# Kernel optimization log

Measured on AMD Instinct MI355X. Metric: run time of the kernel, lower is better.

Reference implementation:

```python
import jax, jax.numpy as jnp
import numpy as np

B, S, H = 4, 8192, 576
I = 512   # moe_intermediate_size
E = 8     # num routed experts
TOP_K = 2

def setup_inputs() -> dict:
    key = jax.random.key(0)
    ks = jax.random.split(key, 8)
    sc = lambda fan_in: 1.0 / np.sqrt(fan_in)
    return {
        'x': jax.random.normal(ks[0], (B, S, H), dtype=jnp.float32),
        'shared_gate_w': jax.random.normal(ks[1], (H, I), dtype=jnp.float32) * sc(H),
        'shared_up_w':   jax.random.normal(ks[2], (H, I), dtype=jnp.float32) * sc(H),
        'shared_down_w': jax.random.normal(ks[3], (I, H), dtype=jnp.float32) * sc(I),
        'routed_gate_w': jax.random.normal(ks[4], (E, H, I), dtype=jnp.float32) * sc(H),
        'routed_up_w':   jax.random.normal(ks[5], (E, H, I), dtype=jnp.float32) * sc(H),
        'routed_down_w': jax.random.normal(ks[6], (E, I, H), dtype=jnp.float32) * sc(I),
        'router_w':      jax.random.normal(ks[7], (H, E), dtype=jnp.float32) * sc(H),
        'router_bias':   jnp.zeros((E,), dtype=jnp.float32),
    }

def reference(x, shared_gate_w, shared_up_w, shared_down_w,
              routed_gate_w, routed_up_w, routed_down_w,
              router_w, router_bias):
    b, s, h = x.shape
    flat = x.reshape(-1, h)                               # [T, H]
    T = flat.shape[0]

    # shared expert (SwiGLU)
    shared = (jax.nn.silu(flat @ shared_gate_w) * (flat @ shared_up_w)) @ shared_down_w

    # router: softmax over experts, top-k, renormalize, scatter back to dense weights
    router_logits = flat @ router_w + router_bias          # [T, E]
    routing_weights = jax.nn.softmax(router_logits, axis=1)
    topk_w, topk_i = jax.lax.top_k(routing_weights, TOP_K)  # [T, k]
    topk_w = topk_w / jnp.sum(topk_w, axis=-1, keepdims=True)
    expert_weights = jnp.zeros((T, routing_weights.shape[1]), dtype=routing_weights.dtype)
    expert_weights = expert_weights.at[jnp.arange(T)[:, None], topk_i].set(topk_w)

    # dense all-expert SwiGLU (faithful to reference: every token through every expert)
    gate = jnp.einsum('th,ehi->tei', flat, routed_gate_w)   # [T, E, I]
    up   = jnp.einsum('th,ehi->tei', flat, routed_up_w)
    expert_out = jnp.einsum('tei,eih->teh', jax.nn.silu(gate) * up, routed_down_w)  # [T, E, H]

    weighted = jnp.einsum('teh,te->th', expert_out, expert_weights)
    return (shared + weighted).reshape(b, s, h)
```

## Files before the change

### kernel.cpp

```cpp
#include <hip/hip_runtime.h>
#include <stdint.h>

#define T_TOK 32768
#define H_DIM 576
#define I_DIM 512
#define NEXP 8
#define WELEM 294912

#define NB_RT 512
#define NB_CW 7776

typedef __attribute__((ext_vector_type(8))) short short8;
typedef __attribute__((ext_vector_type(4))) float f32x4;
typedef __attribute__((ext_vector_type(4))) float f4;
typedef __attribute__((ext_vector_type(4))) unsigned short u16x4;

__device__ __forceinline__ unsigned short f2bf(float f) {
  union { float f; unsigned u; } v; v.f = f;
  unsigned r = (v.u + 0x7fffu + ((v.u >> 16) & 1u)) >> 16;
  return (unsigned short)r;
}

__device__ __forceinline__ void gl16(const void* g, void* l) {
  __builtin_amdgcn_global_load_lds(
      (const __attribute__((address_space(1))) unsigned*)g,
      (__attribute__((address_space(3))) unsigned*)l, 16, 0, 0);
}

__global__ __launch_bounds__(256) void prep_k(
    const float* __restrict__ x, unsigned short* __restrict__ xb,
    const float* __restrict__ rw, const float* __restrict__ rb,
    int* __restrict__ tki, float* __restrict__ tkw, int* __restrict__ counts,
    const float* __restrict__ sgw, const float* __restrict__ suw,
    const float* __restrict__ rgw, const float* __restrict__ ruw,
    const float* __restrict__ sdw, const float* __restrict__ rdw,
    unsigned short* __restrict__ wsg, unsigned short* __restrict__ wsu,
    unsigned short* __restrict__ wrg, unsigned short* __restrict__ wru,
    unsigned short* __restrict__ wsd, unsigned short* __restrict__ wrd) {
  __shared__ __align__(16) char smem[29312];
  int b = blockIdx.x, tid = threadIdx.x;
  if (b < NB_RT) {
    float* lrw = (float*)smem;
    float (*tile)[68] = (float(*)[68])(smem + 18432);
    float (*red)[8] = (float(*)[8])(smem + 27136);
    int* hist = (int*)(smem + 29184);
    for (int i = tid; i < 1152; i += 256)
      *(f4*)&lrw[i * 4] = *(const f4*)&rw[i * 4];
    if (tid < 16) hist[tid] = 0;
    int t0 = b * 64;
    float acc[NEXP] = {};
    for (int c = 0; c < 18; c++) {
      __syncthreads();
#pragma unroll
      for (int k = 0; k < 2; k++) {
        int f = tid + k * 256;
        int rgrp = f >> 8, fl = f & 255;
        int tl2 = fl >> 2, seg = fl & 3;
        int h = rgrp * 288 + c * 16 + seg * 4;
        size_t gi = (size_t)(t0 + tl2) * H_DIM + h;
        f4 v = *(const f4*)(x + gi);
        u16x4 o;
        o.x = f2bf(v.x); o.y = f2bf(v.y); o.z = f2bf(v.z); o.w = f2bf(v.w);
        *(u16x4*)(xb + gi) = o;
        int row = rgrp * 16 + seg * 4;
        tile[row + 0][tl2] = v.x; tile[row + 1][tl2] = v.y;
        tile[row + 2][tl2] = v.z; tile[row + 3][tl2] = v.w;
      }
      __syncthreads();
      if (tid < 128) {
        int half = tid >> 6, tl = tid & 63;
        int hbase = half * 288 + c * 16;
        int rbase = half * 16;
#pragma unroll
        for (int hh = 0; hh < 16; hh++) {
          float xv = tile[rbase + hh][tl];
          f4 w0 = *(const f4*)&lrw[(hbase + hh) * 8];
          f4 w1 = *(const f4*)&lrw[(hbase + hh) * 8 + 4];
          acc[0] += xv * w0.x; acc[1] += xv * w0.y;
          acc[2] += xv * w0.z; acc[3] += xv * w0.w;
          acc[4] += xv * w1.x; acc[5] += xv * w1.y;
          acc[6] += xv * w1.z; acc[7] += xv * w1.w;
        }
      }
    }
    if (tid >= 64 && tid < 128) {
      int tl = tid & 63;
#pragma unroll
      for (int e = 0; e < NEXP; e++) red[tl][e] = acc[e];
    }
    __syncthreads();
    if (tid < 64) {
      int t = t0 + tid;
      float l[NEXP];
#pragma unroll
      for (int e = 0; e < NEXP; e++) l[e] = acc[e] + red[tid][e] + rb[e];
      int e0 = 0;
#pragma unroll
      for (int e = 1; e < NEXP; e++) if (l[e] > l[e0]) e0 = e;
      int e1 = -1;
#pragma unroll
      for (int e = 0; e < NEXP; e++) {
        if (e == e0) continue;
        if (e1 < 0 || l[e] > l[e1]) e1 = e;
      }
      float w0 = 1.f / (1.f + __expf(l[e1] - l[e0]));
      tki[t * 2] = e0; tki[t * 2 + 1] = e1;
      tkw[t * 2] = w0; tkw[t * 2 + 1] = 1.f - w0;
      atomicAdd(&hist[e0], 1);
      atomicAdd(&hist[8 + e1], 1);
    }
    __syncthreads();
    if (tid < 16) atomicAdd(&counts[tid * 32], hist[tid]);
  } else {
    float (*tile)[33] = (float(*)[33])smem;
    int b0 = b - NB_RT;
    const float* src; unsigned short* dst;
    int C, bx, by;
    if (b0 < 5184) {
      int z = b0 / 288, r = b0 % 288;
      bx = r & 15; by = r >> 4; C = 512;
      if (z == 0)      { src = sgw;                            dst = wsg; }
      else if (z == 1) { src = suw;                            dst = wsu; }
      else if (z < 10) { src = rgw + (size_t)(z - 2) * WELEM;  dst = wrg + (size_t)(z - 2) * WELEM; }
      else             { src = ruw + (size_t)(z - 10) * WELEM; dst = wru + (size_t)(z - 10) * WELEM; }
    } else {
      int b2 = b0 - 5184;
      int z = b2 / 288, r = b2 % 288;
      bx = r % 18; by = r / 18; C = 576;
      src = (z == 0) ? sdw : rdw + (size_t)(z - 1) * WELEM;
      dst = (z == 0) ? wsd : wrd + (size_t)(z - 1) * WELEM;
    }
    int R = 1088 - C;
    int tx = tid & 31, ty = tid >> 5;
    int r0 = by * 32, c0 = bx * 32;
    for (int i = ty; i < 32; i += 8)
      tile[i][tx] = src[(size_t)(r0 + i) * C + c0 + tx];
    __syncthreads();
    for (int i = ty; i < 32; i += 8)
      dst[(size_t)(c0 + i) * R + r0 + tx] = f2bf(tile[tx][i]);
  }
}

__global__ void offsets_k(const int* __restrict__ counts, int* __restrict__ offs16,
                          int* __restrict__ pcnt16, int* __restrict__ pinfo) {
  if (threadIdx.x == 0) {
    int o = 0;
    for (int s = 0; s < 16; s++) {
      int c = counts[s * 32];
      int pc = (c + 127) & ~127;
      offs16[s] = o; pcnt16[s] = pc;
      o += pc;
    }
    pinfo[0] = offs16[8];
    pinfo[1] = o - offs16[8];
  }
}

__global__ __launch_bounds__(256) void scatter_k(
    const int* __restrict__ tki, const float* __restrict__ tkw,
    const int* __restrict__ offs16, int* __restrict__ cursor ,
    int* __restrict__ etok, float* __restrict__ ew) {
  __shared__ int hist[16], base[16], lcur[16];
  int tid = threadIdx.x;
  if (tid < 16) { hist[tid] = 0; lcur[tid] = 0; }
  __syncthreads();
  int t = blockIdx.x * 256 + tid;
  int s0 = tki[t * 2], s1 = 8 + tki[t * 2 + 1];
  atomicAdd(&hist[s0], 1);
  atomicAdd(&hist[s1], 1);
  __syncthreads();
  if (tid < 16) base[tid] = atomicAdd(&cursor[tid * 32], hist[tid]);
  __syncthreads();
#pragma unroll
  for (int k = 0; k < 2; k++) {
    int s = (k == 0) ? s0 : s1;
    int r = atomicAdd(&lcur[s], 1);
    int slot = offs16[s] + base[s] + r;
    etok[slot] = t;
    ew[slot] = tkw[t * 2 + k];
  }
}

template <int SHARED>
__global__ __launch_bounds__(512, 2) void gateup_k(
    const unsigned short* __restrict__ xb, const unsigned short* __restrict__ wg,
    const unsigned short* __restrict__ wu, unsigned short* __restrict__ h,
    const int* __restrict__ etok, const int* __restrict__ offs16,
    const int* __restrict__ pcnt16, const int* __restrict__ pinfo,
    int p, int merged, int mchunk) {
  int bid = blockIdx.x;
  int xcd = bid & 7, l = bid >> 3;
  int mb = xcd * mchunk + (l >> 2);
  int nb = l & 3;
  int nrows = SHARED ? T_TOK : (merged ? pinfo[0] + pinfo[1] : pinfo[p]);
  if (mb * 128 >= nrows) return;
  __shared__ unsigned short As[128 * 32];
  __shared__ unsigned short Bg[128 * 32];
  __shared__ unsigned short Bu[128 * 32];
  int t = threadIdx.x;
  int wv = t >> 6, lane = t & 63;
  int ar = t >> 2, seg = t & 3;
  int sg = seg ^ ((ar >> 1) & 3);
  int m0 = mb * 128 + ar;
  int tok0, e = 0;
  if (SHARED) {
    tok0 = m0;
  } else {
    int rl = (!merged && p) ? pinfo[0] : 0;
    int g = rl + m0;
    int s = 0;
#pragma unroll
    for (int i = 0; i < 15; i++) s += (g >= offs16[i] + pcnt16[i]) ? 1 : 0;
    e = s & 7;
    tok0 = etok[g];
    if (tok0 < 0) tok0 = 0;
  }
  const unsigned short* ga = xb + (size_t)tok0 * H_DIM + sg * 8;
  int n0 = nb * 128 + ar;
  const unsigned short* gg = wg + (size_t)e * WELEM + (size_t)n0 * H_DIM + sg * 8;
  const unsigned short* gu = wu + (size_t)e * WELEM + (size_t)n0 * H_DIM + sg * 8;
  char* lA = (char*)As + wv * 1024;
  char* lG = (char*)Bg + wv * 1024;
  char* lU = (char*)Bu + wv * 1024;
  int fr = lane & 15, fq = lane >> 4;
  int wm = (wv >> 2) * 64, wn = (wv & 3) * 32;
  f32x4 accg[4][2] = {};
  f32x4 accu[4][2] = {};
  for (int k0 = 0; k0 < H_DIM; k0 += 32) {
    gl16(ga + k0, lA);
    gl16(gg + k0, lG);
    gl16(gu + k0, lU);
    __syncthreads();
    short8 a[4], g[2], u[2];
#pragma unroll
    for (int i = 0; i < 4; i++) {
      int r = wm + i * 16 + fr;
      a[i] = *(const short8*)&As[r * 32 + (fq ^ ((r >> 1) & 3)) * 8];
    }
#pragma unroll
    for (int j = 0; j < 2; j++) {
      int r = wn + j * 16 + fr;
      int sw = (fq ^ ((r >> 1) & 3)) * 8;
      g[j] = *(const short8*)&Bg[r * 32 + sw];
      u[j] = *(const short8*)&Bu[r * 32 + sw];
    }
#pragma unroll
    for (int i = 0; i < 4; i++)
#pragma unroll
      for (int j = 0; j < 2; j++) {
        accg[i][j] = __builtin_amdgcn_mfma_f32_16x16x32_bf16(a[i], g[j], accg[i][j], 0, 0, 0);
        accu[i][j] = __builtin_amdgcn_mfma_f32_16x16x32_bf16(a[i], u[j], accu[i][j], 0, 0, 0);
      }
    __syncthreads();
  }
#pragma unroll
  for (int i = 0; i < 4; i++)
#pragma unroll
    for (int j = 0; j < 2; j++)
#pragma unroll
      for (int r = 0; r < 4; r++) {
        int row = mb * 128 + wm + i * 16 + fq * 4 + r;
        int col = nb * 128 + wn + j * 16 + fr;
        float gv = accg[i][j][r], uv = accu[i][j][r];
        float hv = (gv / (1.f + __expf(-gv))) * uv;
        h[(size_t)row * I_DIM + col] = f2bf(hv);
      }
}

template <int MODE>
__global__ __launch_bounds__(512, 2) void down_k(
    const unsigned short* __restrict__ hbuf, const unsigned short* __restrict__ wd,
    float* __restrict__ out, const int* __restrict__ etok, const float* __restrict__ ew,
    const int* __restrict__ offs16, const int* __restrict__ pcnt16,
    const int* __restrict__ pinfo, int p, int merged, int mchunk) {
  int bid = blockIdx.x;
  int xcd = bid & 7, l = bid >> 3;
  int mb = xcd * mchunk + l / 3;
  int nb = l % 3;
  int nrows = (MODE == 0) ? T_TOK : pinfo[p];
  if (mb * 128 >= nrows) return;
  int row_lo = (MODE == 1 && p == 1) ? pinfo[0] : 0;
  int hrow_lo = (MODE == 1 && merged) ? row_lo : 0;
  __shared__ char lds[24576];
  unsigned short* Ab = (unsigned short*)lds;
  unsigned short* Bb = (unsigned short*)(lds + 8192);
  int t = threadIdx.x;
  int wv = t >> 6, lane = t & 63;
  int ar = t >> 2, seg = t & 3;
  int sg = seg ^ ((ar >> 1) & 3);
  int e = 0;
  if (MODE == 1) {
    int g = row_lo + mb * 128 + ar;
    int s = 0;
#pragma unroll
    for (int i = 0; i < 15; i++) s += (g >= offs16[i] + pcnt16[i]) ? 1 : 0;
    e = s & 7;
  }
  const unsigned short* ga = hbuf + (size_t)(hrow_lo + mb * 128 + ar) * I_DIM + sg * 8;
  int n00 = nb * 192 + ar;
  const unsigned short* gb0 = wd + (size_t)e * WELEM + (size_t)n00 * I_DIM + sg * 8;
  const unsigned short* gb1 = gb0 + (size_t)128 * I_DIM;
  int wb = wv * 1024;
  int fr = lane & 15, fq = lane >> 4;
  int wm = (wv >> 2) * 64, wn = (wv & 3) * 48;
  f32x4 acc[4][3] = {};
  for (int k0 = 0; k0 < I_DIM; k0 += 32) {
    gl16(ga + k0, (char*)Ab + wb);
    gl16(gb0 + k0, (char*)Bb + wb);
    if (t < 256) gl16(gb1 + k0, (char*)Bb + 8192 + wb);
    __syncthreads();
    short8 a[4], b2[3];
#pragma unroll
    for (int i = 0; i < 4; i++) {
      int r = wm + i * 16 + fr;
      a[i] = *(const short8*)&Ab[r * 32 + (fq ^ ((r >> 1) & 3)) * 8];
    }
#pragma unroll
    for (int j = 0; j < 3; j++) {
      int r = wn + j * 16 + fr;
      b2[j] = *(const short8*)&Bb[r * 32 + (fq ^ ((r >> 1) & 3)) * 8];
    }
#pragma unroll
    for (int i = 0; i < 4; i++)
#pragma unroll
      for (int j = 0; j < 3; j++)
        acc[i][j] = __builtin_amdgcn_mfma_f32_16x16x32_bf16(a[i], b2[j], acc[i][j], 0, 0, 0);
    __syncthreads();
  }
  float* st = (float*)lds;
#pragma unroll
  for (int c = 0; c < 4; c++) {
    __syncthreads();
    if ((wm == 64) == (c >= 2)) {
#pragma unroll
      for (int ii = 0; ii < 2; ii++) {
        int i = (c & 1) * 2 + ii;
#pragma unroll
        for (int j = 0; j < 3; j++)
#pragma unroll
          for (int r = 0; r < 4; r++)
            st[(ii * 16 + fq * 4 + r) * 192 + wn + j * 16 + fr] = acc[i][j][r];
      }
    }
    __syncthreads();
#pragma unroll
    for (int i2 = 0; i2 < 3; i2++) {
      int s = t + i2 * 512;
      int lr = s / 48, qq = s % 48;
      int mloc = mb * 128 + c * 32 + lr;
      int colv = nb * 192 + qq * 4;
      f4 v = *(f4*)&st[lr * 192 + qq * 4];
      if (MODE == 0) {
        *(f4*)&out[(size_t)mloc * H_DIM + colv] = v;
      } else {
        int g = row_lo + mloc;
        int tok = etok[g];
        if (tok >= 0) {
          float w = ew[g];
          float* op = &out[(size_t)tok * H_DIM + colv];
          f4 o = *(f4*)op;
          o.x += w * v.x; o.y += w * v.y; o.z += w * v.z; o.w += w * v.w;
          *(f4*)op = o;
        }
      }
    }
  }
}


extern "C" void kernel_launch(void* const* d_in, const int* in_sizes, int n_in,
                              void* d_out, int out_size, void* d_ws, size_t ws_size,
                              hipStream_t stream) {
  const float* x = (const float*)d_in[0];
  const float* sgw = (const float*)d_in[1];
  const float* suw = (const float*)d_in[2];
  const float* sdw = (const float*)d_in[3];
  const float* rgw = (const float*)d_in[4];
  const float* ruw = (const float*)d_in[5];
  const float* rdw = (const float*)d_in[6];
  const float* rw = (const float*)d_in[7];
  const float* rb = (const float*)d_in[8];
  float* out = (float*)d_out;
  char* ws = (char*)d_ws;

  const size_t o_xb = 0;
  const size_t o_w = 37748736;
  const size_t w_sg = o_w;
  const size_t w_su = o_w + 589824;
  const size_t w_sd = o_w + 1179648;
  const size_t w_rg = o_w + 1769472;
  const size_t w_ru = o_w + 6488064;
  const size_t w_rd = o_w + 11206656;
  const size_t o_tki = o_w + 15925248;
  const size_t o_tkw = o_tki + 262144;
  const size_t o_meta = o_tkw + 262144;
  const size_t o_etok = o_meta + 8192;
  const size_t o_ew = o_etok + 270336;
  const size_t o_h = o_ew + 270336;
  const size_t need_merged = o_h + (size_t)67584 * 1024;

  unsigned short* xb = (unsigned short*)(ws + o_xb);
  int* tki = (int*)(ws + o_tki);
  float* tkw = (float*)(ws + o_tkw);
  int* counts = (int*)(ws + o_meta);
  int* cursor = counts + 512;
  int* offs16 = counts + 1024;
  int* pcnt16 = counts + 1040;
  int* pinfo = counts + 1056;
  int* etok = (int*)(ws + o_etok);
  float* ew = (float*)(ws + o_ew);
  unsigned short* h = (unsigned short*)(ws + o_h);
  int merged = (ws_size >= need_merged) ? 1 : 0;

  unsigned short* wsg = (unsigned short*)(ws + w_sg);
  unsigned short* wsu = (unsigned short*)(ws + w_su);
  unsigned short* wsd = (unsigned short*)(ws + w_sd);
  unsigned short* wrg = (unsigned short*)(ws + w_rg);
  unsigned short* wru = (unsigned short*)(ws + w_ru);
  unsigned short* wrd = (unsigned short*)(ws + w_rd);

  hipMemsetAsync(ws + o_meta, 0, 8192, stream);
  hipMemsetAsync(etok, 0xFF, 270336, stream);

  prep_k<<<NB_RT + NB_CW, 256, 0, stream>>>(
      x, xb, rw, rb, tki, tkw, counts,
      sgw, suw, rgw, ruw, sdw, rdw, wsg, wsu, wrg, wru, wsd, wrd);
  offsets_k<<<1, 64, 0, stream>>>(counts, offs16, pcnt16, pinfo);
  scatter_k<<<128, 256, 0, stream>>>(tki, tkw, offs16, cursor, etok, ew);

  gateup_k<1><<<1024, 512, 0, stream>>>(xb, wsg, wsu, h, nullptr, nullptr,
                                        nullptr, nullptr, 0, 0, 32);
  down_k<0><<<768, 512, 0, stream>>>(h, wsd, out, nullptr, nullptr, nullptr,
                                     nullptr, nullptr, 0, 0, 32);

  if (merged) {
    gateup_k<0><<<2112, 512, 0, stream>>>(xb, wrg, wru, h, etok, offs16,
                                          pcnt16, pinfo, 0, 1, 66);
    down_k<1><<<792, 512, 0, stream>>>(h, wrd, out, etok, ew, offs16,
                                       pcnt16, pinfo, 0, 1, 33);
    down_k<1><<<792, 512, 0, stream>>>(h, wrd, out, etok, ew, offs16,
                                       pcnt16, pinfo, 1, 1, 33);
  } else {
    for (int p = 0; p < 2; p++) {
      gateup_k<0><<<1056, 512, 0, stream>>>(xb, wrg, wru, h, etok, offs16,
                                            pcnt16, pinfo, p, 0, 33);
      down_k<1><<<792, 512, 0, stream>>>(h, wrd, out, etok, ew, offs16,
                                         pcnt16, pinfo, p, 0, 33);
    }
  }
}
```

Measured before the change: 336.9 us.

## Fuse offsets into scatter and merge shared and routed gate-up launches

```diff
diff --git a/kernel.cpp b/kernel.cpp
--- a/kernel.cpp
+++ b/kernel.cpp
@@ -9,6 +9,8 @@
 
 #define NB_RT 512
 #define NB_CW 7776
+#define NB_GU_R 2112
+#define NB_GU_S 1024
 
 typedef __attribute__((ext_vector_type(8))) short short8;
 typedef __attribute__((ext_vector_type(4))) float f32x4;
@@ -141,27 +143,26 @@
   }
 }
 
-__global__ void offsets_k(const int* __restrict__ counts, int* __restrict__ offs16,
-                          int* __restrict__ pcnt16, int* __restrict__ pinfo) {
-  if (threadIdx.x == 0) {
-    int o = 0;
+__global__ __launch_bounds__(256) void scatter_k(
+    const int* __restrict__ tki, const float* __restrict__ tkw,
+    const int* __restrict__ counts, int* __restrict__ cursor ,
+    int* __restrict__ etok, float* __restrict__ ew,
+    int* __restrict__ offs16g, int* __restrict__ pcnt16g,
+    int* __restrict__ pinfog) {
+  __shared__ int soffs[16], hist[16], base[16], lcur[16];
+  int tid = threadIdx.x;
+  if (tid == 0) {
+    int o = 0, p0 = 0;
     for (int s = 0; s < 16; s++) {
       int c = counts[s * 32];
       int pc = (c + 127) & ~127;
-      offs16[s] = o; pcnt16[s] = pc;
+      soffs[s] = o;
+      if (blockIdx.x == 0) { offs16g[s] = o; pcnt16g[s] = pc; }
       o += pc;
-    }
-    pinfo[0] = offs16[8];
-    pinfo[1] = o - offs16[8];
-  }
-}
-
-__global__ __launch_bounds__(256) void scatter_k(
-    const int* __restrict__ tki, const float* __restrict__ tkw,
-    const int* __restrict__ offs16, int* __restrict__ cursor ,
-    int* __restrict__ etok, float* __restrict__ ew) {
-  __shared__ int hist[16], base[16], lcur[16];
-  int tid = threadIdx.x;
+      if (s == 7) p0 = o;
+    }
+    if (blockIdx.x == 0) { pinfog[0] = p0; pinfog[1] = o - p0; }
+  }
   if (tid < 16) { hist[tid] = 0; lcur[tid] = 0; }
   __syncthreads();
   int t = blockIdx.x * 256 + tid;
@@ -175,25 +176,35 @@
   for (int k = 0; k < 2; k++) {
     int s = (k == 0) ? s0 : s1;
     int r = atomicAdd(&lcur[s], 1);
-    int slot = offs16[s] + base[s] + r;
+    int slot = soffs[s] + base[s] + r;
     etok[slot] = t;
     ew[slot] = tkw[t * 2 + k];
   }
 }
 
-template <int SHARED>
 __global__ __launch_bounds__(512, 2) void gateup_k(
-    const unsigned short* __restrict__ xb, const unsigned short* __restrict__ wg,
-    const unsigned short* __restrict__ wu, unsigned short* __restrict__ h,
+    const unsigned short* __restrict__ xb,
+    const unsigned short* __restrict__ wg_s, const unsigned short* __restrict__ wu_s,
+    const unsigned short* __restrict__ wg_r, const unsigned short* __restrict__ wu_r,
+    unsigned short* __restrict__ h_s, unsigned short* __restrict__ h_r,
     const int* __restrict__ etok, const int* __restrict__ offs16,
     const int* __restrict__ pcnt16, const int* __restrict__ pinfo,
-    int p, int merged, int mchunk) {
+    int nrg, int p, int merged, int mchunk_r) {
   int bid = blockIdx.x;
-  int xcd = bid & 7, l = bid >> 3;
-  int mb = xcd * mchunk + (l >> 2);
-  int nb = l & 3;
-  int nrows = SHARED ? T_TOK : (merged ? pinfo[0] + pinfo[1] : pinfo[p]);
-  if (mb * 128 >= nrows) return;
+  bool routed = bid < nrg;
+  int mb, nb;
+  if (routed) {
+    int xcd = bid & 7, l = bid >> 3;
+    mb = xcd * mchunk_r + (l >> 2);
+    nb = l & 3;
+    int nrows = merged ? pinfo[0] + pinfo[1] : pinfo[p];
+    if (mb * 128 >= nrows) return;
+  } else {
+    int b2 = bid - nrg;
+    int xcd = b2 & 7, l = b2 >> 3;
+    mb = xcd * 32 + (l >> 2);
+    nb = l & 3;
+  }
   __shared__ unsigned short As[128 * 32];
   __shared__ unsigned short Bg[128 * 32];
   __shared__ unsigned short Bu[128 * 32];
@@ -202,23 +213,31 @@
   int ar = t >> 2, seg = t & 3;
   int sg = seg ^ ((ar >> 1) & 3);
   int m0 = mb * 128 + ar;
-  int tok0, e = 0;
-  if (SHARED) {
-    tok0 = m0;
-  } else {
+  int tok0;
+  const unsigned short *wgp, *wup;
+  unsigned short* hp;
+  if (routed) {
     int rl = (!merged && p) ? pinfo[0] : 0;
     int g = rl + m0;
     int s = 0;
 #pragma unroll
     for (int i = 0; i < 15; i++) s += (g >= offs16[i] + pcnt16[i]) ? 1 : 0;
-    e = s & 7;
+    int e = s & 7;
     tok0 = etok[g];
     if (tok0 < 0) tok0 = 0;
+    wgp = wg_r + (size_t)e * WELEM;
+    wup = wu_r + (size_t)e * WELEM;
+    hp = h_r;
+  } else {
+    tok0 = m0;
+    wgp = wg_s;
+    wup = wu_s;
+    hp = h_s;
   }
   const unsigned short* ga = xb + (size_t)tok0 * H_DIM + sg * 8;
   int n0 = nb * 128 + ar;
-  const unsigned short* gg = wg + (size_t)e * WELEM + (size_t)n0 * H_DIM + sg * 8;
-  const unsigned short* gu = wu + (size_t)e * WELEM + (size_t)n0 * H_DIM + sg * 8;
+  const unsigned short* gg = wgp + (size_t)n0 * H_DIM + sg * 8;
+  const unsigned short* gu = wup + (size_t)n0 * H_DIM + sg * 8;
   char* lA = (char*)As + wv * 1024;
   char* lG = (char*)Bg + wv * 1024;
   char* lU = (char*)Bu + wv * 1024;
@@ -263,7 +282,7 @@
         int col = nb * 128 + wn + j * 16 + fr;
         float gv = accg[i][j][r], uv = accu[i][j][r];
         float hv = (gv / (1.f + __expf(-gv))) * uv;
-        h[(size_t)row * I_DIM + col] = f2bf(hv);
+        hp[(size_t)row * I_DIM + col] = f2bf(hv);
       }
 }
 
@@ -397,7 +416,9 @@
   const size_t o_etok = o_meta + 8192;
   const size_t o_ew = o_etok + 270336;
   const size_t o_h = o_ew + 270336;
-  const size_t need_merged = o_h + (size_t)67584 * 1024;
+  const size_t o_hS = o_h + (size_t)67584 * 1024;
+  const size_t need_t2 = o_hS;
+  const size_t need_t3 = o_hS + (size_t)32768 * 1024;
 
   unsigned short* xb = (unsigned short*)(ws + o_xb);
   int* tki = (int*)(ws + o_tki);
@@ -410,7 +431,7 @@
   int* etok = (int*)(ws + o_etok);
   float* ew = (float*)(ws + o_ew);
   unsigned short* h = (unsigned short*)(ws + o_h);
-  int merged = (ws_size >= need_merged) ? 1 : 0;
+  unsigned short* hS = (unsigned short*)(ws + o_hS);
 
   unsigned short* wsg = (unsigned short*)(ws + w_sg);
   unsigned short* wsu = (unsigned short*)(ws + w_su);
@@ -425,25 +446,42 @@
   prep_k<<<NB_RT + NB_CW, 256, 0, stream>>>(
       x, xb, rw, rb, tki, tkw, counts,
       sgw, suw, rgw, ruw, sdw, rdw, wsg, wsu, wrg, wru, wsd, wrd);
-  offsets_k<<<1, 64, 0, stream>>>(counts, offs16, pcnt16, pinfo);
-  scatter_k<<<128, 256, 0, stream>>>(tki, tkw, offs16, cursor, etok, ew);
-
-  gateup_k<1><<<1024, 512, 0, stream>>>(xb, wsg, wsu, h, nullptr, nullptr,
-                                        nullptr, nullptr, 0, 0, 32);
-  down_k<0><<<768, 512, 0, stream>>>(h, wsd, out, nullptr, nullptr, nullptr,
-                                     nullptr, nullptr, 0, 0, 32);
-
-  if (merged) {
-    gateup_k<0><<<2112, 512, 0, stream>>>(xb, wrg, wru, h, etok, offs16,
-                                          pcnt16, pinfo, 0, 1, 66);
+  scatter_k<<<128, 256, 0, stream>>>(tki, tkw, counts, cursor, etok, ew,
+                                     offs16, pcnt16, pinfo);
+
+  if (ws_size >= need_t3) {
+    gateup_k<<<NB_GU_R + NB_GU_S, 512, 0, stream>>>(
+        xb, wsg, wsu, wrg, wru, hS, h, etok, offs16, pcnt16, pinfo,
+        NB_GU_R, 0, 1, 66);
+    down_k<0><<<768, 512, 0, stream>>>(hS, wsd, out, nullptr, nullptr, nullptr,
+                                       nullptr, nullptr, 0, 0, 32);
+    down_k<1><<<792, 512, 0, stream>>>(h, wrd, out, etok, ew, offs16,
+                                       pcnt16, pinfo, 0, 1, 33);
+    down_k<1><<<792, 512, 0, stream>>>(h, wrd, out, etok, ew, offs16,
+                                       pcnt16, pinfo, 1, 1, 33);
+  } else if (ws_size >= need_t2) {
+    gateup_k<<<NB_GU_S, 512, 0, stream>>>(
+        xb, wsg, wsu, wrg, wru, h, h, etok, offs16, pcnt16, pinfo,
+        0, 0, 1, 66);
+    down_k<0><<<768, 512, 0, stream>>>(h, wsd, out, nullptr, nullptr, nullptr,
+                                       nullptr, nullptr, 0, 0, 32);
+    gateup_k<<<NB_GU_R, 512, 0, stream>>>(
+        xb, wsg, wsu, wrg, wru, h, h, etok, offs16, pcnt16, pinfo,
+        NB_GU_R, 0, 1, 66);
     down_k<1><<<792, 512, 0, stream>>>(h, wrd, out, etok, ew, offs16,
                                        pcnt16, pinfo, 0, 1, 33);
     down_k<1><<<792, 512, 0, stream>>>(h, wrd, out, etok, ew, offs16,
                                        pcnt16, pinfo, 1, 1, 33);
   } else {
+    gateup_k<<<NB_GU_S, 512, 0, stream>>>(
+        xb, wsg, wsu, wrg, wru, h, h, etok, offs16, pcnt16, pinfo,
+        0, 0, 0, 33);
+    down_k<0><<<768, 512, 0, stream>>>(h, wsd, out, nullptr, nullptr, nullptr,
+                                       nullptr, nullptr, 0, 0, 32);
     for (int p = 0; p < 2; p++) {
-      gateup_k<0><<<1056, 512, 0, stream>>>(xb, wrg, wru, h, etok, offs16,
-                                            pcnt16, pinfo, p, 0, 33);
+      gateup_k<<<1056, 512, 0, stream>>>(
+          xb, wsg, wsu, wrg, wru, h, h, etok, offs16, pcnt16, pinfo,
+          1056, p, 0, 33);
       down_k<1><<<792, 512, 0, stream>>>(h, wrd, out, etok, ew, offs16,
                                          pcnt16, pinfo, p, 0, 33);
     }
```

New measurement: 336.1 us. No clear change (-0.3%).
